# Kernel tuning notes

Measured on AMD Instinct MI355X. Metric: run time of the kernel, lower is better.

Reference implementation:

```python
import jax, jax.numpy as jnp
import numpy as np

D_MODEL = 1024
N_HEADS = 16
HEAD_DIM = D_MODEL // N_HEADS


def setup_inputs() -> dict:
    key = jax.random.key(0)
    k1, k2, k3 = jax.random.split(key, 3)
    x = jax.random.normal(k1, (4, 2048, D_MODEL), dtype=jnp.float32)
    w_qkv = jax.random.normal(k2, (D_MODEL, 3 * D_MODEL), dtype=jnp.float32) * (D_MODEL ** -0.5)
    w_proj = jax.random.normal(k3, (D_MODEL, D_MODEL), dtype=jnp.float32) * (D_MODEL ** -0.5)
    return {"x": x, "w_qkv": w_qkv, "w_proj": w_proj}


def reference(x, w_qkv, w_proj):
    B, T, C = x.shape
    qkv = x @ w_qkv                      # [B,T,3C]
    q, k, v = jnp.split(qkv, 3, axis=-1)
    # [B,T,H,Dh] -> [B,H,T,Dh]
    q = q.reshape(B, T, N_HEADS, HEAD_DIM).transpose(0, 2, 1, 3)
    k = k.reshape(B, T, N_HEADS, HEAD_DIM).transpose(0, 2, 1, 3)
    v = v.reshape(B, T, N_HEADS, HEAD_DIM).transpose(0, 2, 1, 3)
    scale = 1.0 / jnp.sqrt(jnp.asarray(HEAD_DIM, dtype=x.dtype))
    attn = jnp.einsum('bhqd,bhkd->bhqk', q, k) * scale   # [B,H,T,T]
    causal = jnp.tril(jnp.ones((T, T), dtype=bool))
    attn = jnp.where(causal[None, None], attn, jnp.asarray(-jnp.inf, dtype=attn.dtype))
    attn = jax.nn.softmax(attn, axis=-1)
    out = jnp.einsum('bhqk,bhkd->bhqd', attn, v)          # [B,H,T,Dh]
    out = out.transpose(0, 2, 1, 3).reshape(B, T, C)
    return out @ w_proj
```

## Files before the change

### kernel.cpp

```cpp
#include <hip/hip_runtime.h>
#include <hip/hip_bf16.h>
#include <stdint.h>

#define D_MODEL 1024
#define N_HEADS 16
#define HEAD_DIM 64
#define B_SZ 4
#define T_SEQ 2048
#define BH_TOT (B_SZ * N_HEADS)
#define M_ROWS (B_SZ * T_SEQ)

typedef float floatx4 __attribute__((ext_vector_type(4)));
typedef __bf16 bf16x8 __attribute__((ext_vector_type(8)));

__device__ inline unsigned short f2bf(float f) {
  union { float f; unsigned int u; } c; c.f = f;
  unsigned int u = c.u;
  unsigned int r = (u + 0x7FFFu + ((u >> 16) & 1u)) >> 16;
  return (unsigned short)r;
}

__device__ inline unsigned short bfc(float f) {
  return __builtin_bit_cast(unsigned short, (__bf16)f);
}

__device__ __forceinline__ void gload16(const unsigned short* g,
                                        unsigned short* l) {
  __builtin_amdgcn_global_load_lds(
      (const __attribute__((address_space(1))) void*)g,
      (__attribute__((address_space(3))) void*)l, 16, 0, 0);
}

__global__ void cvt_f32_bf16(const float* __restrict__ in,
                             unsigned short* __restrict__ out, int n) {
  int i = (blockIdx.x * blockDim.x + threadIdx.x) * 4;
  if (i + 3 < n) {
    float4 v = *(const float4*)(in + i);
    out[i + 0] = f2bf(v.x);
    out[i + 1] = f2bf(v.y);
    out[i + 2] = f2bf(v.z);
    out[i + 3] = f2bf(v.w);
  } else {
    for (; i < n; ++i) out[i] = f2bf(in[i]);
  }
}

__global__ __launch_bounds__(256) void cvt_transpose(
    const float* __restrict__ in, unsigned short* __restrict__ out,
    int K, int N) {
  __shared__ unsigned short tile[32][33];
  const int n0 = blockIdx.x * 32;
  const int k0 = blockIdx.y * 32;
  const int tx = threadIdx.x & 31;
  const int ty = threadIdx.x >> 5;
#pragma unroll
  for (int r = ty; r < 32; r += 8)
    tile[r][tx] = f2bf(in[(size_t)(k0 + r) * N + n0 + tx]);
  __syncthreads();
#pragma unroll
  for (int r = ty; r < 32; r += 8)
    out[(size_t)(n0 + r) * K + k0 + tx] = tile[tx][r];
}

__global__ __launch_bounds__(256) void transpose_v(
    const unsigned short* __restrict__ Vb, unsigned short* __restrict__ Vt) {
  __shared__ unsigned short tile[32][33];
  const int t0 = blockIdx.x * 32;
  const int d0 = blockIdx.y * 32;
  const int bh = blockIdx.z;
  const unsigned short* src = Vb + (size_t)bh * T_SEQ * HEAD_DIM;
  unsigned short* dst = Vt + (size_t)bh * HEAD_DIM * T_SEQ;
  const int tx = threadIdx.x & 31;
  const int ty = threadIdx.x >> 5;
#pragma unroll
  for (int r = ty; r < 32; r += 8)
    tile[r][tx] = src[(size_t)(t0 + r) * HEAD_DIM + d0 + tx];
  __syncthreads();
#pragma unroll
  for (int r = ty; r < 32; r += 8)
    dst[(size_t)(d0 + r) * T_SEQ + t0 + tx] = tile[tx][r];
}

#define QSCALE 0.1803368801111204f
template <int EPI>
__global__ __launch_bounds__(256) void gemm_bf16(
    const unsigned short* __restrict__ A,
    const unsigned short* __restrict__ Bt, int M, int N, int K,
    unsigned short* __restrict__ Qb, unsigned short* __restrict__ Kb,
    unsigned short* __restrict__ Vb, float* __restrict__ Cout) {
  const int bn = blockIdx.x * 128;
  const int bm = blockIdx.y * 128;
  const int tid = threadIdx.x;
  const int lane = tid & 63;
  const int w = tid >> 6;
  const int wr = w >> 1, wc = w & 1;
  const int l15 = lane & 15;
  const int lg = lane >> 4;

  __shared__ unsigned short As[128 * 32];
  __shared__ unsigned short Bs[128 * 32];

  floatx4 acc[4][4] = {};

  const int srow = w * 16 + (lane >> 2);
  const int scol = (lane & 3) * 8;

  for (int k0 = 0; k0 < K; k0 += 32) {
    gload16(&A[(size_t)(bm + srow) * K + k0 + scol], &As[w * 512]);
    gload16(&A[(size_t)(bm + 64 + srow) * K + k0 + scol], &As[2048 + w * 512]);
    gload16(&Bt[(size_t)(bn + srow) * K + k0 + scol], &Bs[w * 512]);
    gload16(&Bt[(size_t)(bn + 64 + srow) * K + k0 + scol], &Bs[2048 + w * 512]);

    __syncthreads();

    bf16x8 af[4], bfr[4];
#pragma unroll
    for (int mt = 0; mt < 4; ++mt)
      af[mt] = *(const bf16x8*)&As[(wr * 64 + mt * 16 + l15) * 32 + lg * 8];
#pragma unroll
    for (int nt = 0; nt < 4; ++nt)
      bfr[nt] = *(const bf16x8*)&Bs[(wc * 64 + nt * 16 + l15) * 32 + lg * 8];
#pragma unroll
    for (int mt = 0; mt < 4; ++mt)
#pragma unroll
      for (int nt = 0; nt < 4; ++nt)
        acc[mt][nt] = __builtin_amdgcn_mfma_f32_16x16x32_bf16(
            af[mt], bfr[nt], acc[mt][nt], 0, 0, 0);

    __syncthreads();
  }

#pragma unroll
  for (int mt = 0; mt < 4; ++mt)
#pragma unroll
    for (int nt = 0; nt < 4; ++nt)
#pragma unroll
      for (int i = 0; i < 4; ++i) {
        int m = bm + wr * 64 + mt * 16 + lg * 4 + i;
        int n = bn + wc * 64 + nt * 16 + l15;
        float v = acc[mt][nt][i];
        if (EPI == 0) {
          int b = m >> 11;
          int t = m & (T_SEQ - 1);
          int part = n >> 10;
          int nn = n & (D_MODEL - 1);
          int h = nn >> 6;
          int dh = nn & 63;
          size_t idx = ((size_t)(b * N_HEADS + h) * T_SEQ + t) * HEAD_DIM + dh;
          if (part == 0)
            Qb[idx] = bfc(v * QSCALE);
          else if (part == 1)
            Kb[idx] = bfc(v);
          else
            Vb[idx] = bfc(v);
        } else {
          Cout[(size_t)m * N + n] = v;
        }
      }
}

__global__ __launch_bounds__(256) void attn_fwd(
    const unsigned short* __restrict__ Qb, const unsigned short* __restrict__ Kb,
    const unsigned short* __restrict__ Vt, unsigned short* __restrict__ Ob) {
  const int head = blockIdx.x;
  const int p = blockIdx.y;
  const int tid = threadIdx.x;
  const int wid = tid >> 6;
  const int lane = tid & 63;
  const int l15 = lane & 15;
  const int lg = lane >> 4;
  const int b = head >> 4;
  const int h = head & 15;

  const unsigned short* Qh = Qb + (size_t)head * T_SEQ * HEAD_DIM;
  const unsigned short* Kh = Kb + (size_t)head * T_SEQ * HEAD_DIM;
  const unsigned short* Vh = Vt + (size_t)head * HEAD_DIM * T_SEQ;

  __shared__ unsigned short Ks[64 * 72];
  __shared__ unsigned short Vs[64 * 72];
  __shared__ unsigned short Plds[4][2][16][72];

  const int st_row = tid >> 2;
  const int st_col = (tid & 3) * 16;

  for (int ph = 0; ph < 2; ++ph) {
    const int rbase = (ph == 0) ? p * 128 : 2048 - 128 * (p + 1);
    const int nst = (ph == 0) ? 2 * p + 2 : 32 - 2 * p;
    const int q0 = rbase + wid * 32;

    bf16x8 qf[2][2];
#pragma unroll
    for (int t = 0; t < 2; ++t)
#pragma unroll
      for (int c = 0; c < 2; ++c)
        qf[t][c] = *(const bf16x8*)&Qh[(size_t)(q0 + t * 16 + l15) * 64 +
                                       c * 32 + lg * 8];

    floatx4 o[2][4] = {};
    float m_run[2][4], l_part[2][4];
#pragma unroll
    for (int t = 0; t < 2; ++t)
#pragma unroll
      for (int i = 0; i < 4; ++i) {
        m_run[t][i] = -1e30f;
        l_part[t][i] = 0.f;
      }

    uint4 ka, kb2, va, vb2;
    {
      const uint4* gk = (const uint4*)&Kh[(size_t)st_row * 64 + st_col];
      ka = gk[0]; kb2 = gk[1];
      const uint4* gv = (const uint4*)&Vh[(size_t)st_row * T_SEQ + st_col];
      va = gv[0]; vb2 = gv[1];
    }

    for (int kb = 0; kb < nst; ++kb) {
      const int kbase = kb * 64;
      *(uint4*)&Ks[st_row * 72 + st_col] = ka;
      *(uint4*)&Ks[st_row * 72 + st_col + 8] = kb2;
      *(uint4*)&Vs[st_row * 72 + st_col] = va;
      *(uint4*)&Vs[st_row * 72 + st_col + 8] = vb2;
      if (kb + 1 < nst) {
        const int nb = kbase + 64;
        const uint4* gk = (const uint4*)&Kh[(size_t)(nb + st_row) * 64 + st_col];
        ka = gk[0]; kb2 = gk[1];
        const uint4* gv = (const uint4*)&Vh[(size_t)st_row * T_SEQ + nb + st_col];
        va = gv[0]; vb2 = gv[1];
      }
      __syncthreads();

      if (kbase <= q0 + 31) {
        bf16x8 kf0[4], kf1[4];
#pragma unroll
        for (int c = 0; c < 4; ++c) {
          kf0[c] = *(const bf16x8*)&Ks[(c * 16 + l15) * 72 + lg * 8];
          kf1[c] = *(const bf16x8*)&Ks[(c * 16 + l15) * 72 + 32 + lg * 8];
        }
        bf16x8 vf[2][4];
#pragma unroll
        for (int kc = 0; kc < 2; ++kc)
#pragma unroll
          for (int d = 0; d < 4; ++d)
            vf[kc][d] =
                *(const bf16x8*)&Vs[(d * 16 + l15) * 72 + kc * 32 + lg * 8];

        floatx4 s[2][4] = {};
        __builtin_amdgcn_s_setprio(1);
#pragma unroll
        for (int c = 0; c < 4; ++c) {
          s[0][c] = __builtin_amdgcn_mfma_f32_16x16x32_bf16(qf[0][0], kf0[c], s[0][c], 0, 0, 0);
          s[0][c] = __builtin_amdgcn_mfma_f32_16x16x32_bf16(qf[0][1], kf1[c], s[0][c], 0, 0, 0);
          s[1][c] = __builtin_amdgcn_mfma_f32_16x16x32_bf16(qf[1][0], kf0[c], s[1][c], 0, 0, 0);
          s[1][c] = __builtin_amdgcn_mfma_f32_16x16x32_bf16(qf[1][1], kf1[c], s[1][c], 0, 0, 0);
        }
        __builtin_amdgcn_s_setprio(0);

        const int kq = kbase - q0;
        const bool needmask = (kbase + 63 > q0);
#pragma unroll
        for (int t = 0; t < 2; ++t) {
          if (needmask) {
#pragma unroll
            for (int i = 0; i < 4; ++i) {
              int qoff = t * 16 + lg * 4 + i;
#pragma unroll
              for (int c = 0; c < 4; ++c)
                if (c * 16 + l15 + kq > qoff) s[t][c][i] = -1e30f;
            }
          }

          float lmax[4];
          bool need = false;
#pragma unroll
          for (int i = 0; i < 4; ++i) {
            lmax[i] = fmaxf(fmaxf(s[t][0][i], s[t][1][i]),
                            fmaxf(s[t][2][i], s[t][3][i]));
            need |= (lmax[i] > m_run[t][i] + 8.0f);
          }
          if (__any(need)) {
#pragma unroll
            for (int i = 0; i < 4; ++i) {
              float pm = lmax[i];
              pm = fmaxf(pm, __shfl_xor(pm, 1));
              pm = fmaxf(pm, __shfl_xor(pm, 2));
              pm = fmaxf(pm, __shfl_xor(pm, 4));
              pm = fmaxf(pm, __shfl_xor(pm, 8));
              float mnew = fmaxf(m_run[t][i], pm);
              float alpha = exp2f(m_run[t][i] - mnew);
              m_run[t][i] = mnew;
              l_part[t][i] *= alpha;
              o[t][0][i] *= alpha;
              o[t][1][i] *= alpha;
              o[t][2][i] *= alpha;
              o[t][3][i] *= alpha;
            }
          }
#pragma unroll
          for (int i = 0; i < 4; ++i) {
#pragma unroll
            for (int c = 0; c < 4; ++c)
              s[t][c][i] = exp2f(s[t][c][i] - m_run[t][i]);
            l_part[t][i] += (s[t][0][i] + s[t][1][i]) + (s[t][2][i] + s[t][3][i]);
#pragma unroll
            for (int c = 0; c < 4; ++c)
              Plds[wid][t][lg * 4 + i][c * 16 + l15] = bfc(s[t][c][i]);
          }
        }

        __builtin_amdgcn_s_setprio(1);
#pragma unroll
        for (int t = 0; t < 2; ++t) {
          bf16x8 pf0 = *(const bf16x8*)&Plds[wid][t][l15][lg * 8];
          bf16x8 pf1 = *(const bf16x8*)&Plds[wid][t][l15][32 + lg * 8];
#pragma unroll
          for (int d = 0; d < 4; ++d) {
            o[t][d] = __builtin_amdgcn_mfma_f32_16x16x32_bf16(pf0, vf[0][d], o[t][d], 0, 0, 0);
            o[t][d] = __builtin_amdgcn_mfma_f32_16x16x32_bf16(pf1, vf[1][d], o[t][d], 0, 0, 0);
          }
        }
        __builtin_amdgcn_s_setprio(0);
      }

      __syncthreads();
    }

#pragma unroll
    for (int t = 0; t < 2; ++t)
#pragma unroll
      for (int i = 0; i < 4; ++i) {
        float l = l_part[t][i];
        l += __shfl_xor(l, 1);
        l += __shfl_xor(l, 2);
        l += __shfl_xor(l, 4);
        l += __shfl_xor(l, 8);
        float inv = 1.0f / l;
        int q = q0 + t * 16 + lg * 4 + i;
        size_t base = ((size_t)(b * T_SEQ + q)) * D_MODEL + h * HEAD_DIM;
#pragma unroll
        for (int d = 0; d < 4; ++d)
          Ob[base + d * 16 + l15] = bfc(o[t][d][i] * inv);
      }
  }
}

extern "C" void kernel_launch(void* const* d_in, const int* in_sizes, int n_in,
                              void* d_out, int out_size, void* d_ws,
                              size_t ws_size, hipStream_t stream) {
  const float* x = (const float*)d_in[0];
  const float* w_qkv = (const float*)d_in[1];
  const float* w_proj = (const float*)d_in[2];
  float* out = (float*)d_out;

  char* ws = (char*)d_ws;
  size_t off = 0;
  unsigned short* x_bf = (unsigned short*)(ws + off);
  off += (size_t)M_ROWS * D_MODEL * 2;
  unsigned short* wqkv_t = (unsigned short*)(ws + off);
  off += (size_t)D_MODEL * 3 * D_MODEL * 2;
  unsigned short* wproj_t = (unsigned short*)(ws + off);
  off += (size_t)D_MODEL * D_MODEL * 2;
  unsigned short* Qb = (unsigned short*)(ws + off);
  off += (size_t)BH_TOT * T_SEQ * HEAD_DIM * 2;
  unsigned short* Kb = (unsigned short*)(ws + off);
  off += (size_t)BH_TOT * T_SEQ * HEAD_DIM * 2;
  unsigned short* Vb = (unsigned short*)(ws + off);
  off += (size_t)BH_TOT * T_SEQ * HEAD_DIM * 2;
  unsigned short* Vt = (unsigned short*)(ws + off);
  off += (size_t)BH_TOT * T_SEQ * HEAD_DIM * 2;
  unsigned short* Ob = (unsigned short*)(ws + off);
  off += (size_t)M_ROWS * D_MODEL * 2;

  int n1 = M_ROWS * D_MODEL;
  cvt_f32_bf16<<<(n1 / 4 + 255) / 256, 256, 0, stream>>>(x, x_bf, n1);
  cvt_transpose<<<dim3(3 * D_MODEL / 32, D_MODEL / 32), 256, 0, stream>>>(
      w_qkv, wqkv_t, D_MODEL, 3 * D_MODEL);
  cvt_transpose<<<dim3(D_MODEL / 32, D_MODEL / 32), 256, 0, stream>>>(
      w_proj, wproj_t, D_MODEL, D_MODEL);

  gemm_bf16<0><<<dim3(3 * D_MODEL / 128, M_ROWS / 128), 256, 0, stream>>>(
      x_bf, wqkv_t, M_ROWS, 3 * D_MODEL, D_MODEL, Qb, Kb, Vb, nullptr);

  transpose_v<<<dim3(T_SEQ / 32, HEAD_DIM / 32, BH_TOT), 256, 0, stream>>>(Vb, Vt);

  attn_fwd<<<dim3(BH_TOT, 8), 256, 0, stream>>>(Qb, Kb, Vt, Ob);

  gemm_bf16<1><<<dim3(D_MODEL / 128, M_ROWS / 128), 256, 0, stream>>>(
      Ob, wproj_t, M_ROWS, D_MODEL, D_MODEL, nullptr, nullptr, nullptr, out);
}
```

Before: 229.5 us.

## Double-buffer K/V shared tiles and use XOR-swizzled LDS layout

Replaces the padded K, V and P LDS tiles with unpadded 64-wide rows addressed through an XOR swizzle so row reads and writes avoid bank conflicts without padding. K/V tiles are double-buffered: the next tile is written into the alternate buffer after compute, which removes one __syncthreads per iteration. The aim is to cut barrier stalls and LDS conflicts, at the cost of twice the K/V LDS footprint, which may lower occupancy.

```diff
diff --git a/kernel.cpp b/kernel.cpp
--- a/kernel.cpp
+++ b/kernel.cpp
@@ -176,12 +176,16 @@
   const unsigned short* Kh = Kb + (size_t)head * T_SEQ * HEAD_DIM;
   const unsigned short* Vh = Vt + (size_t)head * HEAD_DIM * T_SEQ;
 
-  __shared__ unsigned short Ks[64 * 72];
-  __shared__ unsigned short Vs[64 * 72];
-  __shared__ unsigned short Plds[4][2][16][72];
+  __shared__ unsigned short Ks[2][64 * 64];
+  __shared__ unsigned short Vs[2][64 * 64];
+  __shared__ unsigned short Plds[4][2][16 * 64];
 
   const int st_row = tid >> 2;
-  const int st_col = (tid & 3) * 16;
+  const int st_s0 = (tid & 3) * 2;
+  const int st_r7 = st_row & 7;
+  const int wAddr0 = st_row * 64 + ((st_s0 ^ st_r7) << 3);
+  const int wAddr1 = st_row * 64 + (((st_s0 + 1) ^ st_r7) << 3);
+  const int l7 = l15 & 7;
 
   for (int ph = 0; ph < 2; ++ph) {
     const int rbase = (ph == 0) ? p * 128 : 2048 - 128 * (p + 1);
@@ -208,41 +212,50 @@
 
     uint4 ka, kb2, va, vb2;
     {
-      const uint4* gk = (const uint4*)&Kh[(size_t)st_row * 64 + st_col];
+      const uint4* gk = (const uint4*)&Kh[(size_t)st_row * 64 + (tid & 3) * 16];
       ka = gk[0]; kb2 = gk[1];
-      const uint4* gv = (const uint4*)&Vh[(size_t)st_row * T_SEQ + st_col];
+      const uint4* gv = (const uint4*)&Vh[(size_t)st_row * T_SEQ + (tid & 3) * 16];
       va = gv[0]; vb2 = gv[1];
     }
-
+    __syncthreads();
+    *(uint4*)&Ks[0][wAddr0] = ka;
+    *(uint4*)&Ks[0][wAddr1] = kb2;
+    *(uint4*)&Vs[0][wAddr0] = va;
+    *(uint4*)&Vs[0][wAddr1] = vb2;
+
+    int cur = 0;
     for (int kb = 0; kb < nst; ++kb) {
       const int kbase = kb * 64;
-      *(uint4*)&Ks[st_row * 72 + st_col] = ka;
-      *(uint4*)&Ks[st_row * 72 + st_col + 8] = kb2;
-      *(uint4*)&Vs[st_row * 72 + st_col] = va;
-      *(uint4*)&Vs[st_row * 72 + st_col + 8] = vb2;
-      if (kb + 1 < nst) {
+      __syncthreads();
+
+      const bool more = (kb + 1 < nst);
+      if (more) {
         const int nb = kbase + 64;
-        const uint4* gk = (const uint4*)&Kh[(size_t)(nb + st_row) * 64 + st_col];
+        const uint4* gk =
+            (const uint4*)&Kh[(size_t)(nb + st_row) * 64 + (tid & 3) * 16];
         ka = gk[0]; kb2 = gk[1];
-        const uint4* gv = (const uint4*)&Vh[(size_t)st_row * T_SEQ + nb + st_col];
+        const uint4* gv =
+            (const uint4*)&Vh[(size_t)st_row * T_SEQ + nb + (tid & 3) * 16];
         va = gv[0]; vb2 = gv[1];
       }
-      __syncthreads();
 
       if (kbase <= q0 + 31) {
+        const unsigned short* Kc = Ks[cur];
+        const unsigned short* Vc = Vs[cur];
         bf16x8 kf0[4], kf1[4];
 #pragma unroll
         for (int c = 0; c < 4; ++c) {
-          kf0[c] = *(const bf16x8*)&Ks[(c * 16 + l15) * 72 + lg * 8];
-          kf1[c] = *(const bf16x8*)&Ks[(c * 16 + l15) * 72 + 32 + lg * 8];
+          kf0[c] = *(const bf16x8*)&Kc[(c * 16 + l15) * 64 + ((lg ^ l7) << 3)];
+          kf1[c] =
+              *(const bf16x8*)&Kc[(c * 16 + l15) * 64 + (((4 + lg) ^ l7) << 3)];
         }
         bf16x8 vf[2][4];
 #pragma unroll
         for (int kc = 0; kc < 2; ++kc)
 #pragma unroll
           for (int d = 0; d < 4; ++d)
-            vf[kc][d] =
-                *(const bf16x8*)&Vs[(d * 16 + l15) * 72 + kc * 32 + lg * 8];
+            vf[kc][d] = *(const bf16x8*)&Vc[(d * 16 + l15) * 64 +
+                                            (((kc * 4 + lg) ^ l7) << 3)];
 
         floatx4 s[2][4] = {};
         __builtin_amdgcn_s_setprio(1);
@@ -295,23 +308,29 @@
               o[t][3][i] *= alpha;
             }
           }
+          unsigned short* Pw = Plds[wid][t];
 #pragma unroll
           for (int i = 0; i < 4; ++i) {
 #pragma unroll
             for (int c = 0; c < 4; ++c)
               s[t][c][i] = exp2f(s[t][c][i] - m_run[t][i]);
             l_part[t][i] += (s[t][0][i] + s[t][1][i]) + (s[t][2][i] + s[t][3][i]);
-#pragma unroll
-            for (int c = 0; c < 4; ++c)
-              Plds[wid][t][lg * 4 + i][c * 16 + l15] = bfc(s[t][c][i]);
+            const int prow = lg * 4 + i;
+#pragma unroll
+            for (int c = 0; c < 4; ++c) {
+              int slot = c * 2 + (l15 >> 3);
+              Pw[prow * 64 + (((slot ^ (prow & 7)) << 3) + l7)] =
+                  bfc(s[t][c][i]);
+            }
           }
         }
 
         __builtin_amdgcn_s_setprio(1);
 #pragma unroll
         for (int t = 0; t < 2; ++t) {
-          bf16x8 pf0 = *(const bf16x8*)&Plds[wid][t][l15][lg * 8];
-          bf16x8 pf1 = *(const bf16x8*)&Plds[wid][t][l15][32 + lg * 8];
+          const unsigned short* Pr = Plds[wid][t];
+          bf16x8 pf0 = *(const bf16x8*)&Pr[l15 * 64 + ((lg ^ l7) << 3)];
+          bf16x8 pf1 = *(const bf16x8*)&Pr[l15 * 64 + (((4 + lg) ^ l7) << 3)];
 #pragma unroll
           for (int d = 0; d < 4; ++d) {
             o[t][d] = __builtin_amdgcn_mfma_f32_16x16x32_bf16(pf0, vf[0][d], o[t][d], 0, 0, 0);
@@ -321,7 +340,13 @@
         __builtin_amdgcn_s_setprio(0);
       }
 
-      __syncthreads();
+      if (more) {
+        *(uint4*)&Ks[cur ^ 1][wAddr0] = ka;
+        *(uint4*)&Ks[cur ^ 1][wAddr1] = kb2;
+        *(uint4*)&Vs[cur ^ 1][wAddr0] = va;
+        *(uint4*)&Vs[cur ^ 1][wAddr1] = vb2;
+      }
+      cur ^= 1;
     }
 
 #pragma unroll
```

After: 266.5 us. +16.1%, slower.

## Shrink attention query tile to 64 rows per block, doubling grid size

Applied to the files above, without the earlier changes.

Each wave now handles 16 query rows instead of 32, so a block covers 64 rows per phase and the grid doubles from 8 to 16 blocks per head. The goal is more blocks in flight across CUs and fewer registers per wave, which should help occupancy. The cost is that each K/V tile is staged into LDS for only half as many query rows, so LDS traffic and barrier count per unit of work go up. The per-wave early-exit check on fully masked key blocks is gone, since all waves now overlap the diagonal block.

```diff
diff --git a/kernel.cpp b/kernel.cpp
--- a/kernel.cpp
+++ b/kernel.cpp
@@ -178,33 +178,26 @@
 
   __shared__ unsigned short Ks[64 * 72];
   __shared__ unsigned short Vs[64 * 72];
-  __shared__ unsigned short Plds[4][2][16][72];
+  __shared__ unsigned short Plds[4][16 * 72];
 
   const int st_row = tid >> 2;
   const int st_col = (tid & 3) * 16;
 
   for (int ph = 0; ph < 2; ++ph) {
-    const int rbase = (ph == 0) ? p * 128 : 2048 - 128 * (p + 1);
-    const int nst = (ph == 0) ? 2 * p + 2 : 32 - 2 * p;
-    const int q0 = rbase + wid * 32;
-
-    bf16x8 qf[2][2];
-#pragma unroll
-    for (int t = 0; t < 2; ++t)
-#pragma unroll
-      for (int c = 0; c < 2; ++c)
-        qf[t][c] = *(const bf16x8*)&Qh[(size_t)(q0 + t * 16 + l15) * 64 +
-                                       c * 32 + lg * 8];
-
-    floatx4 o[2][4] = {};
-    float m_run[2][4], l_part[2][4];
-#pragma unroll
-    for (int t = 0; t < 2; ++t)
-#pragma unroll
-      for (int i = 0; i < 4; ++i) {
-        m_run[t][i] = -1e30f;
-        l_part[t][i] = 0.f;
-      }
+    const int rbase = (ph == 0) ? p * 64 : 2048 - 64 * (p + 1);
+    const int nst = (ph == 0) ? p + 1 : 32 - p;
+    const int q0 = rbase + wid * 16;
+
+    bf16x8 qf0 = *(const bf16x8*)&Qh[(size_t)(q0 + l15) * 64 + lg * 8];
+    bf16x8 qf1 = *(const bf16x8*)&Qh[(size_t)(q0 + l15) * 64 + 32 + lg * 8];
+
+    floatx4 o[4] = {};
+    float m_run[4], l_part[4];
+#pragma unroll
+    for (int i = 0; i < 4; ++i) {
+      m_run[i] = -1e30f;
+      l_part[i] = 0.f;
+    }
 
     uint4 ka, kb2, va, vb2;
     {
@@ -229,117 +222,105 @@
       }
       __syncthreads();
 
-      if (kbase <= q0 + 31) {
-        bf16x8 kf0[4], kf1[4];
-#pragma unroll
-        for (int c = 0; c < 4; ++c) {
-          kf0[c] = *(const bf16x8*)&Ks[(c * 16 + l15) * 72 + lg * 8];
-          kf1[c] = *(const bf16x8*)&Ks[(c * 16 + l15) * 72 + 32 + lg * 8];
+      bf16x8 kf0[4], kf1[4];
+#pragma unroll
+      for (int c = 0; c < 4; ++c) {
+        kf0[c] = *(const bf16x8*)&Ks[(c * 16 + l15) * 72 + lg * 8];
+        kf1[c] = *(const bf16x8*)&Ks[(c * 16 + l15) * 72 + 32 + lg * 8];
+      }
+      bf16x8 vf[2][4];
+#pragma unroll
+      for (int kc = 0; kc < 2; ++kc)
+#pragma unroll
+        for (int d = 0; d < 4; ++d)
+          vf[kc][d] = *(const bf16x8*)&Vs[(d * 16 + l15) * 72 + kc * 32 + lg * 8];
+
+      floatx4 sc[4] = {};
+      __builtin_amdgcn_s_setprio(1);
+#pragma unroll
+      for (int c = 0; c < 4; ++c) {
+        sc[c] = __builtin_amdgcn_mfma_f32_16x16x32_bf16(qf0, kf0[c], sc[c], 0, 0, 0);
+        sc[c] = __builtin_amdgcn_mfma_f32_16x16x32_bf16(qf1, kf1[c], sc[c], 0, 0, 0);
+      }
+      __builtin_amdgcn_s_setprio(0);
+
+      const int kq = kbase - q0;
+      if (kbase + 63 > q0) {
+#pragma unroll
+        for (int i = 0; i < 4; ++i) {
+          int qoff = lg * 4 + i;
+#pragma unroll
+          for (int c = 0; c < 4; ++c)
+            if (c * 16 + l15 + kq > qoff) sc[c][i] = -1e30f;
         }
-        bf16x8 vf[2][4];
-#pragma unroll
-        for (int kc = 0; kc < 2; ++kc)
-#pragma unroll
-          for (int d = 0; d < 4; ++d)
-            vf[kc][d] =
-                *(const bf16x8*)&Vs[(d * 16 + l15) * 72 + kc * 32 + lg * 8];
-
-        floatx4 s[2][4] = {};
-        __builtin_amdgcn_s_setprio(1);
-#pragma unroll
-        for (int c = 0; c < 4; ++c) {
-          s[0][c] = __builtin_amdgcn_mfma_f32_16x16x32_bf16(qf[0][0], kf0[c], s[0][c], 0, 0, 0);
-          s[0][c] = __builtin_amdgcn_mfma_f32_16x16x32_bf16(qf[0][1], kf1[c], s[0][c], 0, 0, 0);
-          s[1][c] = __builtin_amdgcn_mfma_f32_16x16x32_bf16(qf[1][0], kf0[c], s[1][c], 0, 0, 0);
-          s[1][c] = __builtin_amdgcn_mfma_f32_16x16x32_bf16(qf[1][1], kf1[c], s[1][c], 0, 0, 0);
+      }
+
+      float lmax[4];
+      bool need = false;
+#pragma unroll
+      for (int i = 0; i < 4; ++i) {
+        lmax[i] = fmaxf(fmaxf(sc[0][i], sc[1][i]), fmaxf(sc[2][i], sc[3][i]));
+        need |= (lmax[i] > m_run[i] + 8.0f);
+      }
+      if (__any(need)) {
+#pragma unroll
+        for (int i = 0; i < 4; ++i) {
+          float pm = lmax[i];
+          pm = fmaxf(pm, __shfl_xor(pm, 1));
+          pm = fmaxf(pm, __shfl_xor(pm, 2));
+          pm = fmaxf(pm, __shfl_xor(pm, 4));
+          pm = fmaxf(pm, __shfl_xor(pm, 8));
+          float mnew = fmaxf(m_run[i], pm);
+          float alpha = exp2f(m_run[i] - mnew);
+          m_run[i] = mnew;
+          l_part[i] *= alpha;
+          o[0][i] *= alpha;
+          o[1][i] *= alpha;
+          o[2][i] *= alpha;
+          o[3][i] *= alpha;
         }
-        __builtin_amdgcn_s_setprio(0);
-
-        const int kq = kbase - q0;
-        const bool needmask = (kbase + 63 > q0);
-#pragma unroll
-        for (int t = 0; t < 2; ++t) {
-          if (needmask) {
-#pragma unroll
-            for (int i = 0; i < 4; ++i) {
-              int qoff = t * 16 + lg * 4 + i;
-#pragma unroll
-              for (int c = 0; c < 4; ++c)
-                if (c * 16 + l15 + kq > qoff) s[t][c][i] = -1e30f;
-            }
-          }
-
-          float lmax[4];
-          bool need = false;
-#pragma unroll
-          for (int i = 0; i < 4; ++i) {
-            lmax[i] = fmaxf(fmaxf(s[t][0][i], s[t][1][i]),
-                            fmaxf(s[t][2][i], s[t][3][i]));
-            need |= (lmax[i] > m_run[t][i] + 8.0f);
-          }
-          if (__any(need)) {
-#pragma unroll
-            for (int i = 0; i < 4; ++i) {
-              float pm = lmax[i];
-              pm = fmaxf(pm, __shfl_xor(pm, 1));
-              pm = fmaxf(pm, __shfl_xor(pm, 2));
-              pm = fmaxf(pm, __shfl_xor(pm, 4));
-              pm = fmaxf(pm, __shfl_xor(pm, 8));
-              float mnew = fmaxf(m_run[t][i], pm);
-              float alpha = exp2f(m_run[t][i] - mnew);
-              m_run[t][i] = mnew;
-              l_part[t][i] *= alpha;
-              o[t][0][i] *= alpha;
-              o[t][1][i] *= alpha;
-              o[t][2][i] *= alpha;
-              o[t][3][i] *= alpha;
-            }
-          }
-#pragma unroll
-          for (int i = 0; i < 4; ++i) {
-#pragma unroll
-            for (int c = 0; c < 4; ++c)
-              s[t][c][i] = exp2f(s[t][c][i] - m_run[t][i]);
-            l_part[t][i] += (s[t][0][i] + s[t][1][i]) + (s[t][2][i] + s[t][3][i]);
-#pragma unroll
-            for (int c = 0; c < 4; ++c)
-              Plds[wid][t][lg * 4 + i][c * 16 + l15] = bfc(s[t][c][i]);
-          }
+      }
+      unsigned short* Pw = Plds[wid];
+#pragma unroll
+      for (int i = 0; i < 4; ++i) {
+#pragma unroll
+        for (int c = 0; c < 4; ++c) sc[c][i] = exp2f(sc[c][i] - m_run[i]);
+        l_part[i] += (sc[0][i] + sc[1][i]) + (sc[2][i] + sc[3][i]);
+        const int prow = lg * 4 + i;
+#pragma unroll
+        for (int c = 0; c < 4; ++c)
+          Pw[prow * 72 + c * 16 + l15] = bfc(sc[c][i]);
+      }
+
+      __builtin_amdgcn_s_setprio(1);
+      {
+        const unsigned short* Pr = Plds[wid];
+        bf16x8 pf0 = *(const bf16x8*)&Pr[l15 * 72 + lg * 8];
+        bf16x8 pf1 = *(const bf16x8*)&Pr[l15 * 72 + 32 + lg * 8];
+#pragma unroll
+        for (int d = 0; d < 4; ++d) {
+          o[d] = __builtin_amdgcn_mfma_f32_16x16x32_bf16(pf0, vf[0][d], o[d], 0, 0, 0);
+          o[d] = __builtin_amdgcn_mfma_f32_16x16x32_bf16(pf1, vf[1][d], o[d], 0, 0, 0);
         }
-
-        __builtin_amdgcn_s_setprio(1);
-#pragma unroll
-        for (int t = 0; t < 2; ++t) {
-          bf16x8 pf0 = *(const bf16x8*)&Plds[wid][t][l15][lg * 8];
-          bf16x8 pf1 = *(const bf16x8*)&Plds[wid][t][l15][32 + lg * 8];
-#pragma unroll
-          for (int d = 0; d < 4; ++d) {
-            o[t][d] = __builtin_amdgcn_mfma_f32_16x16x32_bf16(pf0, vf[0][d], o[t][d], 0, 0, 0);
-            o[t][d] = __builtin_amdgcn_mfma_f32_16x16x32_bf16(pf1, vf[1][d], o[t][d], 0, 0, 0);
-          }
-        }
-        __builtin_amdgcn_s_setprio(0);
-      }
+      }
+      __builtin_amdgcn_s_setprio(0);
 
       __syncthreads();
     }
 
 #pragma unroll
-    for (int t = 0; t < 2; ++t)
-#pragma unroll
-      for (int i = 0; i < 4; ++i) {
-        float l = l_part[t][i];
-        l += __shfl_xor(l, 1);
-        l += __shfl_xor(l, 2);
-        l += __shfl_xor(l, 4);
-        l += __shfl_xor(l, 8);
-        float inv = 1.0f / l;
-        int q = q0 + t * 16 + lg * 4 + i;
-        size_t base = ((size_t)(b * T_SEQ + q)) * D_MODEL + h * HEAD_DIM;
-#pragma unroll
-        for (int d = 0; d < 4; ++d)
-          Ob[base + d * 16 + l15] = bfc(o[t][d][i] * inv);
-      }
+    for (int i = 0; i < 4; ++i) {
+      float l = l_part[i];
+      l += __shfl_xor(l, 1);
+      l += __shfl_xor(l, 2);
+      l += __shfl_xor(l, 4);
+      l += __shfl_xor(l, 8);
+      float inv = 1.0f / l;
+      int q = q0 + lg * 4 + i;
+      size_t base = ((size_t)(b * T_SEQ + q)) * D_MODEL + h * HEAD_DIM;
+#pragma unroll
+      for (int d = 0; d < 4; ++d) Ob[base + d * 16 + l15] = bfc(o[d][i] * inv);
+    }
   }
 }
 
@@ -382,7 +363,7 @@
 
   transpose_v<<<dim3(T_SEQ / 32, HEAD_DIM / 32, BH_TOT), 256, 0, stream>>>(Vb, Vt);
 
-  attn_fwd<<<dim3(BH_TOT, 8), 256, 0, stream>>>(Qb, Kb, Vt, Ob);
+  attn_fwd<<<dim3(BH_TOT, 16), 256, 0, stream>>>(Qb, Kb, Vt, Ob);
 
   gemm_bf16<1><<<dim3(D_MODEL / 128, M_ROWS / 128), 256, 0, stream>>>(
       Ob, wproj_t, M_ROWS, D_MODEL, D_MODEL, nullptr, nullptr, nullptr, out);
```

Result: slower. 238.8 us (+4.1%).

## Transpose attention MFMA operands so each lane owns one query row

Applied to the files above, without the earlier changes.

Swaps the MFMA operand order for both QK^T and PV, so the accumulators hold S^T and O^T and each lane owns a single query row. Row max and sum then need only two cross-lane shuffles instead of four per value, and running stats drop from eight scalars to two per tile. P is written to a swizzled LDS buffer in packed 4-element stores instead of scalar 2-byte stores, and output is written as packed pairs. It also uses a hardware exp2 builtin when available and precomputes LDS offsets, at the cost of more intricate indexing that must stay correct.

```diff
diff --git a/kernel.cpp b/kernel.cpp
--- a/kernel.cpp
+++ b/kernel.cpp
@@ -13,6 +13,12 @@
 typedef float floatx4 __attribute__((ext_vector_type(4)));
 typedef __bf16 bf16x8 __attribute__((ext_vector_type(8)));
 
+#if __has_builtin(__builtin_amdgcn_exp2f)
+#define EXP2(x) __builtin_amdgcn_exp2f(x)
+#else
+#define EXP2(x) exp2f(x)
+#endif
+
 __device__ inline unsigned short f2bf(float f) {
   union { float f; unsigned int u; } c; c.f = f;
   unsigned int u = c.u;
@@ -22,6 +28,10 @@
 
 __device__ inline unsigned short bfc(float f) {
   return __builtin_bit_cast(unsigned short, (__bf16)f);
+}
+
+__device__ inline unsigned int pk2(float lo, float hi) {
+  return (unsigned int)bfc(lo) | ((unsigned int)bfc(hi) << 16);
 }
 
 __device__ __forceinline__ void gload16(const unsigned short* g,
@@ -169,6 +179,7 @@
   const int lane = tid & 63;
   const int l15 = lane & 15;
   const int lg = lane >> 4;
+  const int l7 = l15 & 7;
   const int b = head >> 4;
   const int h = head & 15;
 
@@ -178,10 +189,28 @@
 
   __shared__ unsigned short Ks[64 * 72];
   __shared__ unsigned short Vs[64 * 72];
-  __shared__ unsigned short Plds[4][2][16][72];
+  __shared__ unsigned short Ps[4 * 2 * 16 * 64];
 
   const int st_row = tid >> 2;
   const int st_col = (tid & 3) * 16;
+
+  int kfo0[4], kfo1[4], vfo[2][4];
+#pragma unroll
+  for (int c = 0; c < 4; ++c) {
+    kfo0[c] = (c * 16 + l15) * 72 + lg * 8;
+    kfo1[c] = kfo0[c] + 32;
+  }
+#pragma unroll
+  for (int kc = 0; kc < 2; ++kc)
+#pragma unroll
+    for (int d = 0; d < 4; ++d)
+      vfo[kc][d] = (d * 16 + l15) * 72 + kc * 32 + lg * 8;
+  int pwo[4];
+#pragma unroll
+  for (int c = 0; c < 4; ++c)
+    pwo[c] = l15 * 64 + (((2 * c + (lg >> 1)) ^ l7) << 3) + (lg & 1) * 4;
+  const int pro0 = l15 * 64 + (((4 * 0 + lg) ^ l7) << 3);
+  const int pro1 = l15 * 64 + (((4 * 1 + lg) ^ l7) << 3);
 
   for (int ph = 0; ph < 2; ++ph) {
     const int rbase = (ph == 0) ? p * 128 : 2048 - 128 * (p + 1);
@@ -197,14 +226,8 @@
                                        c * 32 + lg * 8];
 
     floatx4 o[2][4] = {};
-    float m_run[2][4], l_part[2][4];
-#pragma unroll
-    for (int t = 0; t < 2; ++t)
-#pragma unroll
-      for (int i = 0; i < 4; ++i) {
-        m_run[t][i] = -1e30f;
-        l_part[t][i] = 0.f;
-      }
+    float m_run[2] = {-1e30f, -1e30f};
+    float l_part[2] = {0.f, 0.f};
 
     uint4 ka, kb2, va, vb2;
     {
@@ -233,89 +256,97 @@
         bf16x8 kf0[4], kf1[4];
 #pragma unroll
         for (int c = 0; c < 4; ++c) {
-          kf0[c] = *(const bf16x8*)&Ks[(c * 16 + l15) * 72 + lg * 8];
-          kf1[c] = *(const bf16x8*)&Ks[(c * 16 + l15) * 72 + 32 + lg * 8];
+          kf0[c] = *(const bf16x8*)&Ks[kfo0[c]];
+          kf1[c] = *(const bf16x8*)&Ks[kfo1[c]];
         }
         bf16x8 vf[2][4];
 #pragma unroll
         for (int kc = 0; kc < 2; ++kc)
 #pragma unroll
-          for (int d = 0; d < 4; ++d)
-            vf[kc][d] =
-                *(const bf16x8*)&Vs[(d * 16 + l15) * 72 + kc * 32 + lg * 8];
-
-        floatx4 s[2][4] = {};
+          for (int d = 0; d < 4; ++d) vf[kc][d] = *(const bf16x8*)&Vs[vfo[kc][d]];
+
+        floatx4 st_[2][4] = {};
         __builtin_amdgcn_s_setprio(1);
 #pragma unroll
         for (int c = 0; c < 4; ++c) {
-          s[0][c] = __builtin_amdgcn_mfma_f32_16x16x32_bf16(qf[0][0], kf0[c], s[0][c], 0, 0, 0);
-          s[0][c] = __builtin_amdgcn_mfma_f32_16x16x32_bf16(qf[0][1], kf1[c], s[0][c], 0, 0, 0);
-          s[1][c] = __builtin_amdgcn_mfma_f32_16x16x32_bf16(qf[1][0], kf0[c], s[1][c], 0, 0, 0);
-          s[1][c] = __builtin_amdgcn_mfma_f32_16x16x32_bf16(qf[1][1], kf1[c], s[1][c], 0, 0, 0);
+          st_[0][c] = __builtin_amdgcn_mfma_f32_16x16x32_bf16(kf0[c], qf[0][0], st_[0][c], 0, 0, 0);
+          st_[0][c] = __builtin_amdgcn_mfma_f32_16x16x32_bf16(kf1[c], qf[0][1], st_[0][c], 0, 0, 0);
+          st_[1][c] = __builtin_amdgcn_mfma_f32_16x16x32_bf16(kf0[c], qf[1][0], st_[1][c], 0, 0, 0);
+          st_[1][c] = __builtin_amdgcn_mfma_f32_16x16x32_bf16(kf1[c], qf[1][1], st_[1][c], 0, 0, 0);
         }
         __builtin_amdgcn_s_setprio(0);
 
-        const int kq = kbase - q0;
-        const bool needmask = (kbase + 63 > q0);
+        if (kbase + 63 > q0) {
+#pragma unroll
+          for (int t = 0; t < 2; ++t) {
+            const int thr = q0 + t * 16 + l15 - kbase;
+#pragma unroll
+            for (int c = 0; c < 4; ++c)
+#pragma unroll
+              for (int i = 0; i < 4; ++i)
+                if (c * 16 + lg * 4 + i > thr) st_[t][c][i] = -1e30f;
+          }
+        }
+
+        float lmax[2];
+        bool need = false;
 #pragma unroll
         for (int t = 0; t < 2; ++t) {
-          if (needmask) {
+          float v0 = fmaxf(fmaxf(st_[t][0][0], st_[t][0][1]),
+                           fmaxf(st_[t][0][2], st_[t][0][3]));
+          float v1 = fmaxf(fmaxf(st_[t][1][0], st_[t][1][1]),
+                           fmaxf(st_[t][1][2], st_[t][1][3]));
+          float v2 = fmaxf(fmaxf(st_[t][2][0], st_[t][2][1]),
+                           fmaxf(st_[t][2][2], st_[t][2][3]));
+          float v3 = fmaxf(fmaxf(st_[t][3][0], st_[t][3][1]),
+                           fmaxf(st_[t][3][2], st_[t][3][3]));
+          lmax[t] = fmaxf(fmaxf(v0, v1), fmaxf(v2, v3));
+          need |= (lmax[t] > m_run[t] + 8.0f);
+        }
+        if (__any(need)) {
+#pragma unroll
+          for (int t = 0; t < 2; ++t) {
+            float pm = lmax[t];
+            pm = fmaxf(pm, __shfl_xor(pm, 16));
+            pm = fmaxf(pm, __shfl_xor(pm, 32));
+            float mnew = fmaxf(m_run[t], pm);
+            float alpha = EXP2(m_run[t] - mnew);
+            m_run[t] = mnew;
+            l_part[t] *= alpha;
+#pragma unroll
+            for (int c = 0; c < 4; ++c) o[t][c] *= alpha;
+          }
+        }
+
+#pragma unroll
+        for (int t = 0; t < 2; ++t) {
+          const int tb = (wid * 2 + t) * 1024;
+          float sum = 0.f;
+#pragma unroll
+          for (int c = 0; c < 4; ++c) {
 #pragma unroll
             for (int i = 0; i < 4; ++i) {
-              int qoff = t * 16 + lg * 4 + i;
-#pragma unroll
-              for (int c = 0; c < 4; ++c)
-                if (c * 16 + l15 + kq > qoff) s[t][c][i] = -1e30f;
+              st_[t][c][i] = EXP2(st_[t][c][i] - m_run[t]);
+              sum += st_[t][c][i];
             }
+            uint2 w;
+            w.x = pk2(st_[t][c][0], st_[t][c][1]);
+            w.y = pk2(st_[t][c][2], st_[t][c][3]);
+            *(uint2*)&Ps[tb + pwo[c]] = w;
           }
-
-          float lmax[4];
-          bool need = false;
-#pragma unroll
-          for (int i = 0; i < 4; ++i) {
-            lmax[i] = fmaxf(fmaxf(s[t][0][i], s[t][1][i]),
-                            fmaxf(s[t][2][i], s[t][3][i]));
-            need |= (lmax[i] > m_run[t][i] + 8.0f);
-          }
-          if (__any(need)) {
-#pragma unroll
-            for (int i = 0; i < 4; ++i) {
-              float pm = lmax[i];
-              pm = fmaxf(pm, __shfl_xor(pm, 1));
-              pm = fmaxf(pm, __shfl_xor(pm, 2));
-              pm = fmaxf(pm, __shfl_xor(pm, 4));
-              pm = fmaxf(pm, __shfl_xor(pm, 8));
-              float mnew = fmaxf(m_run[t][i], pm);
-              float alpha = exp2f(m_run[t][i] - mnew);
-              m_run[t][i] = mnew;
-              l_part[t][i] *= alpha;
-              o[t][0][i] *= alpha;
-              o[t][1][i] *= alpha;
-              o[t][2][i] *= alpha;
-              o[t][3][i] *= alpha;
-            }
-          }
-#pragma unroll
-          for (int i = 0; i < 4; ++i) {
-#pragma unroll
-            for (int c = 0; c < 4; ++c)
-              s[t][c][i] = exp2f(s[t][c][i] - m_run[t][i]);
-            l_part[t][i] += (s[t][0][i] + s[t][1][i]) + (s[t][2][i] + s[t][3][i]);
-#pragma unroll
-            for (int c = 0; c < 4; ++c)
-              Plds[wid][t][lg * 4 + i][c * 16 + l15] = bfc(s[t][c][i]);
-          }
+          l_part[t] += sum;
         }
 
         __builtin_amdgcn_s_setprio(1);
 #pragma unroll
         for (int t = 0; t < 2; ++t) {
-          bf16x8 pf0 = *(const bf16x8*)&Plds[wid][t][l15][lg * 8];
-          bf16x8 pf1 = *(const bf16x8*)&Plds[wid][t][l15][32 + lg * 8];
-#pragma unroll
-          for (int d = 0; d < 4; ++d) {
-            o[t][d] = __builtin_amdgcn_mfma_f32_16x16x32_bf16(pf0, vf[0][d], o[t][d], 0, 0, 0);
-            o[t][d] = __builtin_amdgcn_mfma_f32_16x16x32_bf16(pf1, vf[1][d], o[t][d], 0, 0, 0);
+          const int tb = (wid * 2 + t) * 1024;
+          bf16x8 pb0 = *(const bf16x8*)&Ps[tb + pro0];
+          bf16x8 pb1 = *(const bf16x8*)&Ps[tb + pro1];
+#pragma unroll
+          for (int dt = 0; dt < 4; ++dt) {
+            o[t][dt] = __builtin_amdgcn_mfma_f32_16x16x32_bf16(vf[0][dt], pb0, o[t][dt], 0, 0, 0);
+            o[t][dt] = __builtin_amdgcn_mfma_f32_16x16x32_bf16(vf[1][dt], pb1, o[t][dt], 0, 0, 0);
           }
         }
         __builtin_amdgcn_s_setprio(0);
@@ -325,21 +356,21 @@
     }
 
 #pragma unroll
-    for (int t = 0; t < 2; ++t)
-#pragma unroll
-      for (int i = 0; i < 4; ++i) {
-        float l = l_part[t][i];
-        l += __shfl_xor(l, 1);
-        l += __shfl_xor(l, 2);
-        l += __shfl_xor(l, 4);
-        l += __shfl_xor(l, 8);
-        float inv = 1.0f / l;
-        int q = q0 + t * 16 + lg * 4 + i;
-        size_t base = ((size_t)(b * T_SEQ + q)) * D_MODEL + h * HEAD_DIM;
-#pragma unroll
-        for (int d = 0; d < 4; ++d)
-          Ob[base + d * 16 + l15] = bfc(o[t][d][i] * inv);
+    for (int t = 0; t < 2; ++t) {
+      float l = l_part[t];
+      l += __shfl_xor(l, 16);
+      l += __shfl_xor(l, 32);
+      float inv = 1.0f / l;
+      int q = q0 + t * 16 + l15;
+      size_t base = ((size_t)(b * T_SEQ + q)) * D_MODEL + h * HEAD_DIM;
+#pragma unroll
+      for (int dt = 0; dt < 4; ++dt) {
+        unsigned int u0 = pk2(o[t][dt][0] * inv, o[t][dt][1] * inv);
+        unsigned int u1 = pk2(o[t][dt][2] * inv, o[t][dt][3] * inv);
+        *(unsigned int*)&Ob[base + dt * 16 + lg * 4] = u0;
+        *(unsigned int*)&Ob[base + dt * 16 + lg * 4 + 2] = u1;
       }
+    }
   }
 }
 
```

New measurement: 209.6 us. -8.7%, faster.
